# Optimization experiments

Hardware: AMD Instinct MI355X
Metric: run time of the kernel (lower is better)

The kernel has to match this reference:

```python
import jax, jax.numpy as jnp
import numpy as np
import math

INPUT_SIZE = 1024
HIDDEN_SIZE = 1024
BATCH = 4096


def setup_inputs() -> dict:
    key = jax.random.key(0)
    ks = jax.random.split(key, 16)
    stddev = 1.0 / math.sqrt(HIDDEN_SIZE)

    def unif(k, shape):
        return jax.random.uniform(k, shape, minval=-stddev, maxval=stddev, dtype=jnp.float32)

    inp = {
        'x': jax.random.normal(ks[0], (BATCH, INPUT_SIZE), dtype=jnp.float32),
        'h_prev': jax.random.normal(ks[1], (BATCH, HIDDEN_SIZE), dtype=jnp.float32),
        'c_prev': jax.random.normal(ks[2], (BATCH, HIDDEN_SIZE), dtype=jnp.float32),
        'igx': unif(ks[3], (INPUT_SIZE, HIDDEN_SIZE)),
        'igu': unif(ks[4], (HIDDEN_SIZE, HIDDEN_SIZE)),
        'ib': unif(ks[5], (HIDDEN_SIZE,)),
        'fgx': unif(ks[6], (INPUT_SIZE, HIDDEN_SIZE)),
        'fgu': unif(ks[7], (HIDDEN_SIZE, HIDDEN_SIZE)),
        'fb': unif(ks[8], (HIDDEN_SIZE,)),
        'ogx': unif(ks[9], (INPUT_SIZE, HIDDEN_SIZE)),
        'ogu': unif(ks[10], (HIDDEN_SIZE, HIDDEN_SIZE)),
        'ob': unif(ks[11], (HIDDEN_SIZE,)),
        'cgx': unif(ks[12], (INPUT_SIZE, HIDDEN_SIZE)),
        'cgu': unif(ks[13], (HIDDEN_SIZE, HIDDEN_SIZE)),
        'cb': unif(ks[14], (HIDDEN_SIZE,)),
    }
    return inp


def reference(x, h_prev, c_prev, igx, igu, ib, fgx, fgu, fb, ogx, ogu, ob, cgx, cgu, cb):
    # Fuse the 8 gate matmuls into 2 GEMMs via concatenated weights.
    # Wx: [input_size, 4H], Wh: [hidden, 4H], b: [4H]; gate order i,f,o,c.
    Wx = jnp.concatenate([igx, fgx, ogx, cgx], axis=1)
    Wh = jnp.concatenate([igu, fgu, ogu, cgu], axis=1)
    b = jnp.concatenate([ib, fb, ob, cb], axis=0)
    gates = x @ Wx + h_prev @ Wh + b  # [B, 4H]
    H = c_prev.shape[-1]
    ig = jax.nn.sigmoid(gates[:, 0 * H:1 * H])
    fg = jax.nn.sigmoid(gates[:, 1 * H:2 * H])
    og = jax.nn.sigmoid(gates[:, 2 * H:3 * H])
    cc = jnp.tanh(gates[:, 3 * H:4 * H])
    c = fg * c_prev + ig * cc
    h = og * jnp.tanh(c)
    return (h, c)
```

## Files before the change

kernel.cpp:

```cpp
#include <hip/hip_runtime.h>
#include <hip/hip_bf16.h>

typedef unsigned short u16;
typedef unsigned int u32;
typedef short bf16x8 __attribute__((ext_vector_type(8)));
typedef float f32x4 __attribute__((ext_vector_type(4)));
typedef u16 u16x8 __attribute__((ext_vector_type(8)));

#define HID 1024
#define BATCH 4096
#define KTOT 2048
#define NT 32
#define A0B 0
#define A1B 16384
#define B0B 32768
#define B1B 49152

__device__ __forceinline__ u16 f2bf(float f) {
  u32 v = __builtin_bit_cast(u32, f);
  u32 r = (v + 0x7fffu + ((v >> 16) & 1u)) >> 16;
  return (u16)r;
}
__device__ __forceinline__ float sigmoid_fast(float x) {
  return 1.0f / (1.0f + __expf(-x));
}
__device__ __forceinline__ float tanh_fast(float x) {
  return 2.0f * sigmoid_fast(2.0f * x) - 1.0f;
}
__device__ __forceinline__ void gl_lds16(const void* g, void* l) {
  __builtin_amdgcn_global_load_lds(
      (const __attribute__((address_space(1))) u32*)g,
      (__attribute__((address_space(3))) u32*)l, 16, 0, 0);
}

__global__ __launch_bounds__(256) void prep_all(
    const float* __restrict__ x, const float* __restrict__ hp,
    const float* __restrict__ igx, const float* __restrict__ fgx,
    const float* __restrict__ ogx, const float* __restrict__ cgx,
    const float* __restrict__ igu, const float* __restrict__ fgu,
    const float* __restrict__ ogu, const float* __restrict__ cgu,
    u16* __restrict__ xh, u16* __restrict__ bt) {
  __shared__ u16 lds[64 * 66];
  if (blockIdx.x < 4096) {
    int c = blockIdx.x * 256 + threadIdx.x;
    int row = c >> 8;
    int col0 = (c & 255) << 3;
    const float* src = (col0 < 1024)
                           ? (x + (size_t)row * 1024 + col0)
                           : (hp + (size_t)row * 1024 + (col0 - 1024));
    f32x4 a = *(const f32x4*)(src);
    f32x4 b = *(const f32x4*)(src + 4);
    u16x8 v;
#pragma unroll
    for (int j = 0; j < 4; ++j) { v[j] = f2bf(a[j]); v[j + 4] = f2bf(b[j]); }
    *(u16x8*)(xh + (size_t)row * KTOT + col0) = v;
    return;
  }
  const float* srcs[8] = {igx, fgx, ogx, cgx, igu, fgu, ogu, cgu};
  int bid = blockIdx.x - 4096;
  int m = bid >> 8;
  int tile = bid & 255;
  int th = tile & 15, tk = tile >> 4;
  int h0 = th << 6, k0 = tk << 6;
  int g = m & 3, which = m >> 2;
  const float* W = srcs[m] + (size_t)k0 * HID + h0;

  int t = threadIdx.x;
  int r1 = t >> 4;
  int c1 = (t & 15) << 2;
#pragma unroll
  for (int p = 0; p < 4; ++p) {
    int row = (p << 4) + r1;
    f32x4 v = *(const f32x4*)(W + (size_t)row * HID + c1);
    u32 p0 = (u32)f2bf(v[0]) | ((u32)f2bf(v[1]) << 16);
    u32 p1 = (u32)f2bf(v[2]) | ((u32)f2bf(v[3]) << 16);
    u32* d = (u32*)&lds[row * 66 + c1];
    d[0] = p0;
    d[1] = p1;
  }
  __syncthreads();
  int nl = t >> 2;
  int kc = t & 3;
  int row_np = ((h0 >> 4) << 6) + ((nl >> 4) << 6) + (g << 4) + (nl & 15);
  size_t dst = (size_t)row_np * KTOT + (size_t)which * 1024 + k0;
  u16x8 a2, b2;
#pragma unroll
  for (int j = 0; j < 8; ++j) {
    a2[j] = lds[(kc * 8 + j) * 66 + nl];
    b2[j] = lds[(kc * 8 + 32 + j) * 66 + nl];
  }
  *(u16x8*)(&bt[dst + kc * 8]) = a2;
  *(u16x8*)(&bt[dst + kc * 8 + 32]) = b2;
}

__global__ __launch_bounds__(512, 2) void lstm_gemm(
    const u16* __restrict__ xh, const u16* __restrict__ bt,
    const float* __restrict__ cprev,
    const float* __restrict__ ib, const float* __restrict__ fb,
    const float* __restrict__ ob, const float* __restrict__ cb,
    float* __restrict__ hout, float* __restrict__ cout) {
  __shared__ __align__(16) u16 lds[4 * 16384];

  int sx = threadIdx.x;
  int bid = blockIdx.x;
  int xcd = bid & 7, lid = bid >> 3;
  int brow = ((xcd & 3) << 2) | (lid & 3);
  int bcol = ((xcd >> 2) << 3) | (lid >> 2);

  int w = sx >> 6, l = sx & 63;
  int wr = (w >> 2) << 7;
  int wc = (w & 3) << 6;
  int lrow = l & 15, q = l >> 4;
  int grow = brow << 8;

  int prow = sx >> 3;
  int koff = ((sx & 7) ^ (prow & 7)) << 3;
  const u16* aS0 = xh + (size_t)(grow + prow) * KTOT + koff;
  const u16* aS1 = aS0 + (size_t)128 * KTOT;
  const u16* bS0 = bt + (size_t)(bcol * 256 + prow) * KTOT + koff;
  const u16* bS1 = bS0 + (size_t)128 * KTOT;
  int sx8 = sx * 8;

  int aoff = (wr + lrow) << 6;
  int boff = (wc + lrow) << 6;
  int pc0 = (q ^ (lrow & 7)) << 3;
  int pc1 = ((q + 4) ^ (lrow & 7)) << 3;

  f32x4 acc[8][4] = {};
  bf16x8 af0[2][2], af1[2][2], af2[2][2];
  bf16x8 bfr[4][2];

#define STG(P_, K_, D_)                                                       \
  gl_lds16((P_) + (K_), &lds[(D_) + sx8]);                                    \
  gl_lds16((P_) + (size_t)64 * KTOT + (K_), &lds[(D_) + 4096 + sx8]);

#define RDA(AB_, i, pc) (*(const bf16x8*)&lds[(AB_) + aoff + (i) * 1024 + (pc)])
#define RDB(BB_, j, pc) (*(const bf16x8*)&lds[(BB_) + boff + (j) * 1024 + (pc)])

#define ISS_A(D_, AB_, I0_)                                                   \
  D_[0][0] = RDA(AB_, I0_, pc0);                                              \
  D_[0][1] = RDA(AB_, I0_, pc1);                                              \
  D_[1][0] = RDA(AB_, (I0_) + 1, pc0);                                        \
  D_[1][1] = RDA(AB_, (I0_) + 1, pc1);

#define ISS_B(D_, BB_)                                                        \
  D_[0][0] = RDB(BB_, 0, pc0); D_[0][1] = RDB(BB_, 0, pc1);                   \
  D_[1][0] = RDB(BB_, 1, pc0); D_[1][1] = RDB(BB_, 1, pc1);                   \
  D_[2][0] = RDB(BB_, 2, pc0); D_[2][1] = RDB(BB_, 2, pc1);                   \
  D_[3][0] = RDB(BB_, 3, pc0); D_[3][1] = RDB(BB_, 3, pc1);

#define MFMA16(K_, AF_)                                                       \
  _Pragma("unroll") for (int s2 = 0; s2 < 2; ++s2) {                          \
    _Pragma("unroll") for (int j = 0; j < 4; ++j) {                           \
      acc[2 * (K_)][j] = __builtin_amdgcn_mfma_f32_16x16x32_bf16(             \
          AF_[0][s2], bfr[j][s2], acc[2 * (K_)][j], 0, 0, 0);                 \
      acc[2 * (K_) + 1][j] = __builtin_amdgcn_mfma_f32_16x16x32_bf16(         \
          AF_[1][s2], bfr[j][s2], acc[2 * (K_) + 1][j], 0, 0, 0);             \
    }                                                                         \
  }

#define INTERIOR(AC_, BC_)                                                    \
  ISS_B(bfr, (BC_))                                                           \
  ISS_A(af0, (AC_), 0)                                                        \
  ISS_A(af1, (AC_), 2)                                                        \
  MFMA16(0, af0)                                                              \
  ISS_A(af2, (AC_), 4)                                                        \
  MFMA16(1, af1)                                                              \
  ISS_A(af0, (AC_), 6)                                                        \
  MFMA16(2, af2)                                                              \
  MFMA16(3, af0)

#define TILE(AC_, BC_, KN_, AD_, BD_)                                         \
  {                                                                           \
    STG(aS0, (KN_), (AD_))                                                    \
    STG(aS1, (KN_), (AD_) + 8192)                                             \
    STG(bS0, (KN_), (BD_))                                                    \
    STG(bS1, (KN_), (BD_) + 8192)                                             \
    __builtin_amdgcn_sched_barrier(0);                                        \
    INTERIOR(AC_, BC_)                                                        \
  }

  STG(aS0, 0, A0B)
  STG(aS1, 0, A0B + 8192)
  STG(bS0, 0, B0B)
  STG(bS1, 0, B0B + 8192)
  __syncthreads();

  for (int tp = 0; tp < 15; ++tp) {
    int k1 = (2 * tp + 1) << 6;
    int k2 = (2 * tp + 2) << 6;
    TILE(A0B, B0B, k1, A1B, B1B)
    __syncthreads();
    TILE(A1B, B1B, k2, A0B, B0B)
    __syncthreads();
  }
  TILE(A0B, B0B, 31 << 6, A1B, B1B)
  __syncthreads();
  INTERIOR(A1B, B1B)

#undef TILE
#undef INTERIOR
#undef MFMA16
#undef ISS_A
#undef ISS_B
#undef RDA
#undef RDB
#undef STG

  int sb = (bcol << 2) + (w & 3);
  int hcol = (sb << 4) + lrow;
  float bi = ib[hcol];
  float bff = fb[hcol];
  float bo = ob[hcol];
  float bc = cb[hcol];

#pragma unroll
  for (int i = 0; i < 8; ++i) {
    int row0 = grow + wr + i * 16 + q * 4;
#pragma unroll
    for (int r = 0; r < 4; ++r) {
      size_t idx = (size_t)(row0 + r) * HID + hcol;
      float gi = sigmoid_fast(acc[i][0][r] + bi);
      float gf = sigmoid_fast(acc[i][1][r] + bff);
      float go = sigmoid_fast(acc[i][2][r] + bo);
      float gc = tanh_fast(acc[i][3][r] + bc);
      float cp = cprev[idx];
      float cv = gf * cp + gi * gc;
      hout[idx] = go * tanh_fast(cv);
      cout[idx] = cv;
    }
  }
}

extern "C" void kernel_launch(void* const* d_in, const int* in_sizes, int n_in,
                              void* d_out, int out_size, void* d_ws, size_t ws_size,
                              hipStream_t stream) {
  const float* x   = (const float*)d_in[0];
  const float* hp  = (const float*)d_in[1];
  const float* cp  = (const float*)d_in[2];
  const float* igx = (const float*)d_in[3];
  const float* igu = (const float*)d_in[4];
  const float* ib  = (const float*)d_in[5];
  const float* fgx = (const float*)d_in[6];
  const float* fgu = (const float*)d_in[7];
  const float* fb  = (const float*)d_in[8];
  const float* ogx = (const float*)d_in[9];
  const float* ogu = (const float*)d_in[10];
  const float* ob  = (const float*)d_in[11];
  const float* cgx = (const float*)d_in[12];
  const float* cgu = (const float*)d_in[13];
  const float* cb  = (const float*)d_in[14];

  u16* bt = (u16*)d_ws;
  u16* xh = bt + (size_t)4096 * 2048;
  float* hout = (float*)d_out;
  float* cout = hout + (size_t)BATCH * HID;

  prep_all<<<6144, 256, 0, stream>>>(x, hp, igx, fgx, ogx, cgx,
                                     igu, fgu, ogu, cgu, xh, bt);
  lstm_gemm<<<256, 512, 0, stream>>>(xh, bt, cp, ib, fb, ob, cb,
                                     hout, cout);
}
```

Before: 208.3 us.

## Switch GEMM inner loop to 32x32x16 MFMA with shuffle-based gate epilogue

After: 208.8 us. Within noise of the previous version (+0.3%).

```diff
diff --git a/kernel.cpp b/kernel.cpp
--- a/kernel.cpp
+++ b/kernel.cpp
@@ -5,6 +5,7 @@
 typedef unsigned int u32;
 typedef short bf16x8 __attribute__((ext_vector_type(8)));
 typedef float f32x4 __attribute__((ext_vector_type(4)));
+typedef float f32x16 __attribute__((ext_vector_type(16)));
 typedef u16 u16x8 __attribute__((ext_vector_type(8)));
 
 #define HID 1024
@@ -110,7 +111,6 @@
   int w = sx >> 6, l = sx & 63;
   int wr = (w >> 2) << 7;
   int wc = (w & 3) << 6;
-  int lrow = l & 15, q = l >> 4;
   int grow = brow << 8;
 
   int prow = sx >> 3;
@@ -121,54 +121,56 @@
   const u16* bS1 = bS0 + (size_t)128 * KTOT;
   int sx8 = sx * 8;
 
-  int aoff = (wr + lrow) << 6;
-  int boff = (wc + lrow) << 6;
-  int pc0 = (q ^ (lrow & 7)) << 3;
-  int pc1 = ((q + 4) ^ (lrow & 7)) << 3;
-
-  f32x4 acc[8][4] = {};
-  bf16x8 af0[2][2], af1[2][2], af2[2][2];
-  bf16x8 bfr[4][2];
+  int l31 = l & 31, hi = l >> 5, side = (l >> 4) & 1;
+  int arow_l = (wr + l31) << 6;
+  int brow_l = (wc + l31) << 6;
+  int pk0 = ((0 + hi) ^ (l & 7)) << 3;
+  int pk1 = ((2 + hi) ^ (l & 7)) << 3;
+  int pk2 = ((4 + hi) ^ (l & 7)) << 3;
+  int pk3 = ((6 + hi) ^ (l & 7)) << 3;
+
+  f32x16 acc[4][2] = {};
+  bf16x8 af0[4], af1[4];
+  bf16x8 bfr[2][4];
 
 #define STG(P_, K_, D_)                                                       \
   gl_lds16((P_) + (K_), &lds[(D_) + sx8]);                                    \
   gl_lds16((P_) + (size_t)64 * KTOT + (K_), &lds[(D_) + 4096 + sx8]);
 
-#define RDA(AB_, i, pc) (*(const bf16x8*)&lds[(AB_) + aoff + (i) * 1024 + (pc)])
-#define RDB(BB_, j, pc) (*(const bf16x8*)&lds[(BB_) + boff + (j) * 1024 + (pc)])
-
-#define ISS_A(D_, AB_, I0_)                                                   \
-  D_[0][0] = RDA(AB_, I0_, pc0);                                              \
-  D_[0][1] = RDA(AB_, I0_, pc1);                                              \
-  D_[1][0] = RDA(AB_, (I0_) + 1, pc0);                                        \
-  D_[1][1] = RDA(AB_, (I0_) + 1, pc1);
-
-#define ISS_B(D_, BB_)                                                        \
-  D_[0][0] = RDB(BB_, 0, pc0); D_[0][1] = RDB(BB_, 0, pc1);                   \
-  D_[1][0] = RDB(BB_, 1, pc0); D_[1][1] = RDB(BB_, 1, pc1);                   \
-  D_[2][0] = RDB(BB_, 2, pc0); D_[2][1] = RDB(BB_, 2, pc1);                   \
-  D_[3][0] = RDB(BB_, 3, pc0); D_[3][1] = RDB(BB_, 3, pc1);
-
-#define MFMA16(K_, AF_)                                                       \
-  _Pragma("unroll") for (int s2 = 0; s2 < 2; ++s2) {                          \
-    _Pragma("unroll") for (int j = 0; j < 4; ++j) {                           \
-      acc[2 * (K_)][j] = __builtin_amdgcn_mfma_f32_16x16x32_bf16(             \
-          AF_[0][s2], bfr[j][s2], acc[2 * (K_)][j], 0, 0, 0);                 \
-      acc[2 * (K_) + 1][j] = __builtin_amdgcn_mfma_f32_16x16x32_bf16(         \
-          AF_[1][s2], bfr[j][s2], acc[2 * (K_) + 1][j], 0, 0, 0);             \
+#define ISS_A(D_, AC_, M_)                                                    \
+  D_[0] = *(const bf16x8*)&lds[(AC_) + arow_l + (M_) * 2048 + pk0];           \
+  D_[1] = *(const bf16x8*)&lds[(AC_) + arow_l + (M_) * 2048 + pk1];           \
+  D_[2] = *(const bf16x8*)&lds[(AC_) + arow_l + (M_) * 2048 + pk2];           \
+  D_[3] = *(const bf16x8*)&lds[(AC_) + arow_l + (M_) * 2048 + pk3];
+
+#define ISS_B(BC_)                                                            \
+  bfr[0][0] = *(const bf16x8*)&lds[(BC_) + brow_l + pk0];                     \
+  bfr[0][1] = *(const bf16x8*)&lds[(BC_) + brow_l + pk1];                     \
+  bfr[0][2] = *(const bf16x8*)&lds[(BC_) + brow_l + pk2];                     \
+  bfr[0][3] = *(const bf16x8*)&lds[(BC_) + brow_l + pk3];                     \
+  bfr[1][0] = *(const bf16x8*)&lds[(BC_) + brow_l + 2048 + pk0];              \
+  bfr[1][1] = *(const bf16x8*)&lds[(BC_) + brow_l + 2048 + pk1];              \
+  bfr[1][2] = *(const bf16x8*)&lds[(BC_) + brow_l + 2048 + pk2];              \
+  bfr[1][3] = *(const bf16x8*)&lds[(BC_) + brow_l + 2048 + pk3];
+
+#define MFMA8(M_, AF_)                                                        \
+  _Pragma("unroll") for (int n = 0; n < 2; ++n) {                             \
+    _Pragma("unroll") for (int ks = 0; ks < 4; ++ks) {                        \
+      acc[M_][n] = __builtin_amdgcn_mfma_f32_32x32x16_bf16(                   \
+          AF_[ks], bfr[n][ks], acc[M_][n], 0, 0, 0);                          \
     }                                                                         \
   }
 
 #define INTERIOR(AC_, BC_)                                                    \
-  ISS_B(bfr, (BC_))                                                           \
+  ISS_B((BC_))                                                                \
   ISS_A(af0, (AC_), 0)                                                        \
-  ISS_A(af1, (AC_), 2)                                                        \
-  MFMA16(0, af0)                                                              \
-  ISS_A(af2, (AC_), 4)                                                        \
-  MFMA16(1, af1)                                                              \
-  ISS_A(af0, (AC_), 6)                                                        \
-  MFMA16(2, af2)                                                              \
-  MFMA16(3, af0)
+  ISS_A(af1, (AC_), 1)                                                        \
+  MFMA8(0, af0)                                                               \
+  ISS_A(af0, (AC_), 2)                                                        \
+  MFMA8(1, af1)                                                               \
+  ISS_A(af1, (AC_), 3)                                                        \
+  MFMA8(2, af0)                                                               \
+  MFMA8(3, af1)
 
 #define TILE(AC_, BC_, KN_, AD_, BD_)                                         \
   {                                                                           \
@@ -200,30 +202,38 @@
 
 #undef TILE
 #undef INTERIOR
-#undef MFMA16
+#undef MFMA8
 #undef ISS_A
 #undef ISS_B
-#undef RDA
-#undef RDB
 #undef STG
 
-  int sb = (bcol << 2) + (w & 3);
-  int hcol = (sb << 4) + lrow;
+  int hcol = ((bcol << 2) + (w & 3)) * 16 + (l31 & 15);
   float bi = ib[hcol];
   float bff = fb[hcol];
   float bo = ob[hcol];
   float bc = cb[hcol];
 
 #pragma unroll
-  for (int i = 0; i < 8; ++i) {
-    int row0 = grow + wr + i * 16 + q * 4;
-#pragma unroll
-    for (int r = 0; r < 4; ++r) {
-      size_t idx = (size_t)(row0 + r) * HID + hcol;
-      float gi = sigmoid_fast(acc[i][0][r] + bi);
-      float gf = sigmoid_fast(acc[i][1][r] + bff);
-      float go = sigmoid_fast(acc[i][2][r] + bo);
-      float gc = tanh_fast(acc[i][3][r] + bc);
+  for (int m = 0; m < 4; ++m) {
+    int rowb = grow + wr + m * 32 + 4 * hi + (side ? 16 : 0);
+#pragma unroll
+    for (int rr = 0; rr < 8; ++rr) {
+      float o_lo0 = acc[m][0][rr], o_hi0 = acc[m][0][rr + 8];
+      float o_lo1 = acc[m][1][rr], o_hi1 = acc[m][1][rr + 8];
+      float r_lo0 = __shfl_xor(o_lo0, 16, 64);
+      float r_hi0 = __shfl_xor(o_hi0, 16, 64);
+      float r_lo1 = __shfl_xor(o_lo1, 16, 64);
+      float r_hi1 = __shfl_xor(o_hi1, 16, 64);
+      float iv = side ? r_hi0 : o_lo0;
+      float fv = side ? o_hi0 : r_lo0;
+      float ov = side ? r_hi1 : o_lo1;
+      float gv = side ? o_hi1 : r_lo1;
+      int row = rowb + (rr & 3) + 8 * (rr >> 2);
+      size_t idx = (size_t)row * HID + hcol;
+      float gi = sigmoid_fast(iv + bi);
+      float gf = sigmoid_fast(fv + bff);
+      float go = sigmoid_fast(ov + bo);
+      float gc = tanh_fast(gv + bc);
       float cp = cprev[idx];
       float cv = gf * cp + gi * gc;
       hout[idx] = go * tanh_fast(cv);
```

## Shrink GEMM block tile to 256x128 with BK=32 and 4 waves

Applied to the files above, without the earlier changes.

Result: slower. 213.6 us (+2.6%).

```diff
diff --git a/kernel.cpp b/kernel.cpp
--- a/kernel.cpp
+++ b/kernel.cpp
@@ -10,11 +10,11 @@
 #define HID 1024
 #define BATCH 4096
 #define KTOT 2048
-#define NT 32
+#define NT 64
 #define A0B 0
-#define A1B 16384
-#define B0B 32768
-#define B1B 49152
+#define A1B 8192
+#define B0B 16384
+#define B1B 20480
 
 __device__ __forceinline__ u16 f2bf(float f) {
   u32 v = __builtin_bit_cast(u32, f);
@@ -93,121 +93,88 @@
   *(u16x8*)(&bt[dst + kc * 8 + 32]) = b2;
 }
 
-__global__ __launch_bounds__(512, 2) void lstm_gemm(
+__global__ __launch_bounds__(256, 2) void lstm_gemm(
     const u16* __restrict__ xh, const u16* __restrict__ bt,
     const float* __restrict__ cprev,
     const float* __restrict__ ib, const float* __restrict__ fb,
     const float* __restrict__ ob, const float* __restrict__ cb,
     float* __restrict__ hout, float* __restrict__ cout) {
-  __shared__ __align__(16) u16 lds[4 * 16384];
+  __shared__ __align__(16) u16 lds[24576];
 
   int sx = threadIdx.x;
   int bid = blockIdx.x;
   int xcd = bid & 7, lid = bid >> 3;
   int brow = ((xcd & 3) << 2) | (lid & 3);
-  int bcol = ((xcd >> 2) << 3) | (lid >> 2);
+  int bcol = ((xcd >> 2) << 4) | (lid >> 2);
 
   int w = sx >> 6, l = sx & 63;
-  int wr = (w >> 2) << 7;
-  int wc = (w & 3) << 6;
+  int wr = (w >> 1) << 7;
+  int wc = (w & 1) << 6;
   int lrow = l & 15, q = l >> 4;
   int grow = brow << 8;
 
-  int prow = sx >> 3;
-  int koff = ((sx & 7) ^ (prow & 7)) << 3;
-  const u16* aS0 = xh + (size_t)(grow + prow) * KTOT + koff;
-  const u16* aS1 = aS0 + (size_t)128 * KTOT;
-  const u16* bS0 = bt + (size_t)(bcol * 256 + prow) * KTOT + koff;
-  const u16* bS1 = bS0 + (size_t)128 * KTOT;
+  int prow = sx >> 2;
+  int koff = ((sx & 3) ^ (prow & 3)) << 3;
+  const u16* aS = xh + (size_t)(grow + prow) * KTOT + koff;
+  const u16* bS = bt + (size_t)(bcol * 128 + prow) * KTOT + koff;
   int sx8 = sx * 8;
 
-  int aoff = (wr + lrow) << 6;
-  int boff = (wc + lrow) << 6;
-  int pc0 = (q ^ (lrow & 7)) << 3;
-  int pc1 = ((q + 4) ^ (lrow & 7)) << 3;
+  int arow_l = (wr + lrow) << 5;
+  int brow_l = (wc + lrow) << 5;
+  int pc = (q ^ (lrow & 3)) << 3;
 
   f32x4 acc[8][4] = {};
-  bf16x8 af0[2][2], af1[2][2], af2[2][2];
-  bf16x8 bfr[4][2];
-
-#define STG(P_, K_, D_)                                                       \
-  gl_lds16((P_) + (K_), &lds[(D_) + sx8]);                                    \
-  gl_lds16((P_) + (size_t)64 * KTOT + (K_), &lds[(D_) + 4096 + sx8]);
-
-#define RDA(AB_, i, pc) (*(const bf16x8*)&lds[(AB_) + aoff + (i) * 1024 + (pc)])
-#define RDB(BB_, j, pc) (*(const bf16x8*)&lds[(BB_) + boff + (j) * 1024 + (pc)])
-
-#define ISS_A(D_, AB_, I0_)                                                   \
-  D_[0][0] = RDA(AB_, I0_, pc0);                                              \
-  D_[0][1] = RDA(AB_, I0_, pc1);                                              \
-  D_[1][0] = RDA(AB_, (I0_) + 1, pc0);                                        \
-  D_[1][1] = RDA(AB_, (I0_) + 1, pc1);
-
-#define ISS_B(D_, BB_)                                                        \
-  D_[0][0] = RDB(BB_, 0, pc0); D_[0][1] = RDB(BB_, 0, pc1);                   \
-  D_[1][0] = RDB(BB_, 1, pc0); D_[1][1] = RDB(BB_, 1, pc1);                   \
-  D_[2][0] = RDB(BB_, 2, pc0); D_[2][1] = RDB(BB_, 2, pc1);                   \
-  D_[3][0] = RDB(BB_, 3, pc0); D_[3][1] = RDB(BB_, 3, pc1);
-
-#define MFMA16(K_, AF_)                                                       \
-  _Pragma("unroll") for (int s2 = 0; s2 < 2; ++s2) {                          \
+  bf16x8 af[8], bfr[4];
+
+#define STG(KK_, AD_, BD_)                                                    \
+  gl_lds16(aS + (KK_), &lds[(AD_) + sx8]);                                    \
+  gl_lds16(aS + (size_t)64 * KTOT + (KK_), &lds[(AD_) + 2048 + sx8]);         \
+  gl_lds16(aS + (size_t)128 * KTOT + (KK_), &lds[(AD_) + 4096 + sx8]);        \
+  gl_lds16(aS + (size_t)192 * KTOT + (KK_), &lds[(AD_) + 6144 + sx8]);        \
+  gl_lds16(bS + (KK_), &lds[(BD_) + sx8]);                                    \
+  gl_lds16(bS + (size_t)64 * KTOT + (KK_), &lds[(BD_) + 2048 + sx8]);
+
+#define INTERIOR(AC_, BC_)                                                    \
+  bfr[0] = *(const bf16x8*)&lds[(BC_) + brow_l + 0 * 512 + pc];               \
+  bfr[1] = *(const bf16x8*)&lds[(BC_) + brow_l + 1 * 512 + pc];               \
+  bfr[2] = *(const bf16x8*)&lds[(BC_) + brow_l + 2 * 512 + pc];               \
+  bfr[3] = *(const bf16x8*)&lds[(BC_) + brow_l + 3 * 512 + pc];               \
+  _Pragma("unroll") for (int i = 0; i < 8; ++i)                               \
+      af[i] = *(const bf16x8*)&lds[(AC_) + arow_l + i * 512 + pc];            \
+  _Pragma("unroll") for (int i = 0; i < 8; ++i) {                             \
     _Pragma("unroll") for (int j = 0; j < 4; ++j) {                           \
-      acc[2 * (K_)][j] = __builtin_amdgcn_mfma_f32_16x16x32_bf16(             \
-          AF_[0][s2], bfr[j][s2], acc[2 * (K_)][j], 0, 0, 0);                 \
-      acc[2 * (K_) + 1][j] = __builtin_amdgcn_mfma_f32_16x16x32_bf16(         \
-          AF_[1][s2], bfr[j][s2], acc[2 * (K_) + 1][j], 0, 0, 0);             \
+      acc[i][j] = __builtin_amdgcn_mfma_f32_16x16x32_bf16(                    \
+          af[i], bfr[j], acc[i][j], 0, 0, 0);                                 \
     }                                                                         \
   }
-
-#define INTERIOR(AC_, BC_)                                                    \
-  ISS_B(bfr, (BC_))                                                           \
-  ISS_A(af0, (AC_), 0)                                                        \
-  ISS_A(af1, (AC_), 2)                                                        \
-  MFMA16(0, af0)                                                              \
-  ISS_A(af2, (AC_), 4)                                                        \
-  MFMA16(1, af1)                                                              \
-  ISS_A(af0, (AC_), 6)                                                        \
-  MFMA16(2, af2)                                                              \
-  MFMA16(3, af0)
 
 #define TILE(AC_, BC_, KN_, AD_, BD_)                                         \
   {                                                                           \
-    STG(aS0, (KN_), (AD_))                                                    \
-    STG(aS1, (KN_), (AD_) + 8192)                                             \
-    STG(bS0, (KN_), (BD_))                                                    \
-    STG(bS1, (KN_), (BD_) + 8192)                                             \
+    STG((KN_), (AD_), (BD_))                                                  \
     __builtin_amdgcn_sched_barrier(0);                                        \
     INTERIOR(AC_, BC_)                                                        \
   }
 
-  STG(aS0, 0, A0B)
-  STG(aS1, 0, A0B + 8192)
-  STG(bS0, 0, B0B)
-  STG(bS1, 0, B0B + 8192)
+  STG(0, A0B, B0B)
   __syncthreads();
 
-  for (int tp = 0; tp < 15; ++tp) {
-    int k1 = (2 * tp + 1) << 6;
-    int k2 = (2 * tp + 2) << 6;
+  for (int tp = 0; tp < 31; ++tp) {
+    int k1 = (2 * tp + 1) << 5;
+    int k2 = (2 * tp + 2) << 5;
     TILE(A0B, B0B, k1, A1B, B1B)
     __syncthreads();
     TILE(A1B, B1B, k2, A0B, B0B)
     __syncthreads();
   }
-  TILE(A0B, B0B, 31 << 6, A1B, B1B)
+  TILE(A0B, B0B, 63 << 5, A1B, B1B)
   __syncthreads();
   INTERIOR(A1B, B1B)
 
 #undef TILE
 #undef INTERIOR
-#undef MFMA16
-#undef ISS_A
-#undef ISS_B
-#undef RDA
-#undef RDB
 #undef STG
 
-  int sb = (bcol << 2) + (w & 3);
+  int sb = (bcol << 1) + (w & 1);
   int hcol = (sb << 4) + lrow;
   float bi = ib[hcol];
   float bff = fb[hcol];
@@ -258,6 +225,6 @@
 
   prep_all<<<6144, 256, 0, stream>>>(x, hp, igx, fgx, ogx, cgx,
                                      igu, fgu, ogu, cgu, xh, bt);
-  lstm_gemm<<<256, 512, 0, stream>>>(xh, bt, cp, ib, fb, ob, cb,
+  lstm_gemm<<<512, 256, 0, stream>>>(xh, bt, cp, ib, fb, ob, cb,
                                      hout, cout);
 }
```
